# Performance work log

Measured on AMD Instinct MI355X. Metric: run time of the kernel, lower is better.

## Reference

```python
import jax, jax.numpy as jnp
import numpy as np

B, L, C = 2, 2048, 1024
H = 16
D = C // H  # 64
ROPE_THETA = 10000.0


def _rope_tables(seq_len, head_dim, dtype=jnp.float32):
    # freqs_cis equivalent: angle[t, j] = t * theta^(-2j/head_dim)
    inv_freq = 1.0 / (ROPE_THETA ** (jnp.arange(0, head_dim, 2, dtype=jnp.float32) / head_dim))
    ang = jnp.arange(seq_len, dtype=jnp.float32)[:, None] * inv_freq[None, :]  # [L, D/2]
    return jnp.cos(ang).astype(dtype), jnp.sin(ang).astype(dtype)


def setup_inputs() -> dict:
    key = jax.random.key(0)
    k1, k2, k3 = jax.random.split(key, 3)
    x = jax.random.normal(k1, (B, L, C), dtype=jnp.float32)
    qkv_w = jax.random.normal(k2, (3 * C, C), dtype=jnp.float32) * 0.02
    proj_w = jax.random.normal(k3, (C, C), dtype=jnp.float32) * 0.02
    proj_b = jnp.zeros((C,), dtype=jnp.float32)
    cos, sin = _rope_tables(L, D)
    return {"x": x, "qkv_w": qkv_w, "proj_w": proj_w, "proj_b": proj_b, "cos": cos, "sin": sin}


def _apply_rope(t, cos, sin):
    # t: [B, L, H, D]; cos/sin: [L, D/2]; interleaved complex rotation
    te = t[..., 0::2]
    to = t[..., 1::2]
    c = cos[None, :, None, :]
    s = sin[None, :, None, :]
    re = te * c - to * s
    im = te * s + to * c
    out = jnp.stack([re, im], axis=-1)  # [B, L, H, D/2, 2]
    return out.reshape(t.shape)


def reference(x, qkv_w, proj_w, proj_b, cos, sin):
    b, l, c = x.shape
    scale = (c // H) ** -0.5
    qkv = (x @ qkv_w.T).reshape(b, l, 3, H, c // H)  # [B, L, 3, H, D]
    q, k, v = qkv[:, :, 0], qkv[:, :, 1], qkv[:, :, 2]  # each [B, L, H, D]
    q = _apply_rope(q, cos, sin)
    k = _apply_rope(k, cos, sin)
    # memory_efficient_attention math: softmax(q k^T * scale) v, per head
    logits = jnp.einsum("blhd,bmhd->bhlm", q, k) * scale  # [B, H, L, L]
    p = jax.nn.softmax(logits, axis=-1)
    out = jnp.einsum("bhlm,bmhd->blhd", p, v).reshape(b, l, c)
    return out @ proj_w.T + proj_b
```

## Files before the change

### kernel.cpp

```cpp
#include <hip/hip_runtime.h>


typedef __attribute__((ext_vector_type(8))) short s8v;
typedef __attribute__((ext_vector_type(4))) float f4v;

__device__ __forceinline__ unsigned short f2bf(float f) {
  unsigned int u = __float_as_uint(f);
  u += 0x7FFFu + ((u >> 16) & 1u);
  return (unsigned short)(u >> 16);
}

__device__ __forceinline__ void gl16(const unsigned short* g, unsigned short* l) {
  __builtin_amdgcn_global_load_lds((const __attribute__((address_space(1))) void*)g,
                                   (__attribute__((address_space(3))) void*)l,
                                   16, 0, 0);
}

__device__ __forceinline__ s8v pack8(const float* p) {
  const float4 a = *reinterpret_cast<const float4*>(p);
  const float4 b = *reinterpret_cast<const float4*>(p + 4);
  s8v r;
  r[0]=(short)f2bf(a.x); r[1]=(short)f2bf(a.y); r[2]=(short)f2bf(a.z); r[3]=(short)f2bf(a.w);
  r[4]=(short)f2bf(b.x); r[5]=(short)f2bf(b.y); r[6]=(short)f2bf(b.z); r[7]=(short)f2bf(b.w);
  return r;
}

__global__ __launch_bounds__(256)
void k_convert(const float* __restrict__ X, const float* __restrict__ W,
               const float* __restrict__ Wp,
               unsigned short* __restrict__ Xb, unsigned short* __restrict__ Wb,
               unsigned short* __restrict__ Wpb)
{
  const int bid = blockIdx.x, tid = threadIdx.x;
  if (bid < 2048) {
    const size_t e = (size_t)bid * 2048 + (size_t)tid * 8;
    *reinterpret_cast<s8v*>(Xb + e) = pack8(X + e);
  } else if (bid < 3584) {
    const size_t e = (size_t)(bid - 2048) * 2048 + (size_t)tid * 8;
    const int p = (int)(e >> 10);
    const int col = (int)(e & 1023);
    int n;
    if (p < 2048) {
      const int t = p >> 10;
      const int hh = (p & 1023) >> 6;
      const int c = p & 63;
      const int d = (c < 32) ? (c << 1) : (((c - 32) << 1) | 1);
      n = (t << 10) + (hh << 6) + d;
    } else {
      n = p;
    }
    *reinterpret_cast<s8v*>(Wb + e) = pack8(W + (size_t)n * 1024 + col);
  } else {
    const size_t e = (size_t)(bid - 3584) * 2048 + (size_t)tid * 8;
    *reinterpret_cast<s8v*>(Wpb + e) = pack8(Wp + e);
  }
}

__global__ __launch_bounds__(256)
void k_gemm_qkv(const unsigned short* __restrict__ Ab,
                const unsigned short* __restrict__ Bb,
                const float* __restrict__ Ct, const float* __restrict__ St,
                unsigned short* __restrict__ qb, unsigned short* __restrict__ kb,
                unsigned short* __restrict__ vb)
{
  __shared__ __align__(16) unsigned short Asm[128 * 32];
  __shared__ __align__(16) unsigned short Bsm[128 * 32];

  const int tid  = threadIdx.x;
  const int w    = tid >> 6;
  const int lane = tid & 63;
  const int lr   = lane & 15;
  const int lg   = lane >> 4;
  const int wm   = w >> 1, wn = w & 1;

  const int row0 = blockIdx.x << 7;
  const int col0 = blockIdx.y << 7;

  const int srow = (w << 5) + (lane >> 2);
  const int scol = (lane & 3) << 3;
  const unsigned short* Ag = Ab + (size_t)(row0 + srow) * 1024 + scol;
  const unsigned short* Bg = Bb + (size_t)(col0 + srow) * 1024 + scol;
  unsigned short* Al0 = &Asm[(w << 5) * 32];
  unsigned short* Al1 = Al0 + 512;
  unsigned short* Bl0 = &Bsm[(w << 5) * 32];
  unsigned short* Bl1 = Bl0 + 512;

  f4v acc[4][4];
#pragma unroll
  for (int m = 0; m < 4; ++m)
#pragma unroll
    for (int n = 0; n < 4; ++n) acc[m][n] = (f4v){0.f, 0.f, 0.f, 0.f};

  for (int k0 = 0; k0 < 1024; k0 += 32) {
    gl16(Ag + k0, Al0);
    gl16(Ag + k0 + 16 * 1024, Al1);
    gl16(Bg + k0, Bl0);
    gl16(Bg + k0 + 16 * 1024, Bl1);
    __syncthreads();

    s8v af[4], bfr[4];
#pragma unroll
    for (int m = 0; m < 4; ++m)
      af[m] = *reinterpret_cast<const s8v*>(&Asm[(wm * 64 + m * 16 + lr) * 32 + lg * 8]);
#pragma unroll
    for (int n = 0; n < 4; ++n)
      bfr[n] = *reinterpret_cast<const s8v*>(&Bsm[(wn * 64 + n * 16 + lr) * 32 + lg * 8]);
#pragma unroll
    for (int m = 0; m < 4; ++m)
#pragma unroll
      for (int n = 0; n < 4; ++n)
        acc[m][n] = __builtin_amdgcn_mfma_f32_16x16x32_bf16(af[m], bfr[n], acc[m][n], 0, 0, 0);
    __syncthreads();
  }

  const int colbase = col0 + wn * 64;
  const int t  = colbase >> 10;
  const int h  = (colbase & 1023) >> 6;
  unsigned short* dst = (t == 0) ? qb : (t == 1) ? kb : vb;
  const float sc = (t == 0) ? 0.125f : 1.0f;

#pragma unroll
  for (int m = 0; m < 4; ++m) {
#pragma unroll
    for (int j = 0; j < 4; ++j) {
      const int token = row0 + wm * 64 + m * 16 + lg * 4 + j;
      const int bI = token >> 11;
      const int lI = token & 2047;
      unsigned short* rowp = dst + (((size_t)bI * 16 + h) * 2048 + lI) * 64;
      if (t == 2) {
#pragma unroll
        for (int n = 0; n < 4; ++n) rowp[n * 16 + lr] = f2bf(acc[m][n][j]);
      } else {
#pragma unroll
        for (int pn = 0; pn < 2; ++pn) {
          const int d2 = pn * 16 + lr;
          const float c = Ct[lI * 32 + d2];
          const float s = St[lI * 32 + d2];
          const float e = acc[m][pn][j];
          const float o = acc[m][pn + 2][j];
          rowp[d2]      = f2bf((e * c - o * s) * sc);
          rowp[32 + d2] = f2bf((e * s + o * c) * sc);
        }
      }
    }
  }
}

__global__ __launch_bounds__(256)
void k_attn(const unsigned short* __restrict__ qb,
            const unsigned short* __restrict__ kb,
            const unsigned short* __restrict__ vb,
            unsigned short* __restrict__ ab)
{
  __shared__ unsigned short Ps[4][16][72];
  __shared__ unsigned short Vt[64][72];

  const int tid  = threadIdx.x;
  const int w    = tid >> 6;
  const int lane = tid & 63;
  const int lr   = lane & 15;
  const int lg   = lane >> 4;

  const int bx = blockIdx.x;
  const int qt = bx & 31;
  const int h  = (bx >> 5) & 15;
  const int b  = bx >> 9;

  const size_t bh = ((size_t)b * 16 + h) * 2048;
  const unsigned short* Qp = qb + (bh + (size_t)qt * 64 + w * 16) * 64;
  const unsigned short* Kp = kb + bh * 64;
  const unsigned short* Vp = vb + bh * 64;

  const s8v qa0 = *reinterpret_cast<const s8v*>(Qp + lr * 64 + 0 + lg * 8);
  const s8v qa1 = *reinterpret_cast<const s8v*>(Qp + lr * 64 + 32 + lg * 8);

  f4v o[4];
#pragma unroll
  for (int i = 0; i < 4; ++i) o[i] = (f4v){0.f, 0.f, 0.f, 0.f};
  float mrow[4] = {-1e30f, -1e30f, -1e30f, -1e30f};
  float lrow[4] = {0.f, 0.f, 0.f, 0.f};

  const int vc = tid >> 2;
  const int vd = (tid & 3) << 4;

  for (int kt = 0; kt < 32; ++kt) {
    const unsigned short* Kt = Kp + (size_t)kt * 64 * 64;
    const unsigned short* Vs = Vp + (size_t)kt * 64 * 64;

    s8v kf[4][2];
#pragma unroll
    for (int ct = 0; ct < 4; ++ct) {
      kf[ct][0] = *reinterpret_cast<const s8v*>(Kt + (ct * 16 + lr) * 64 + 0 + lg * 8);
      kf[ct][1] = *reinterpret_cast<const s8v*>(Kt + (ct * 16 + lr) * 64 + 32 + lg * 8);
    }
    const s8v v0 = *reinterpret_cast<const s8v*>(Vs + vc * 64 + vd);
    const s8v v1 = *reinterpret_cast<const s8v*>(Vs + vc * 64 + vd + 8);

    __syncthreads();
#pragma unroll
    for (int j = 0; j < 8; ++j) {
      Vt[vd + j][vc]     = (unsigned short)v0[j];
      Vt[vd + 8 + j][vc] = (unsigned short)v1[j];
    }

    f4v s[4];
#pragma unroll
    for (int ct = 0; ct < 4; ++ct) {
      f4v z = (f4v){0.f, 0.f, 0.f, 0.f};
      z = __builtin_amdgcn_mfma_f32_16x16x32_bf16(qa0, kf[ct][0], z, 0, 0, 0);
      z = __builtin_amdgcn_mfma_f32_16x16x32_bf16(qa1, kf[ct][1], z, 0, 0, 0);
      s[ct] = z;
    }

    float pexp[4][4];
#pragma unroll
    for (int r = 0; r < 4; ++r) {
      float mx = fmaxf(fmaxf(s[0][r], s[1][r]), fmaxf(s[2][r], s[3][r]));
#pragma unroll
      for (int mk = 1; mk <= 8; mk <<= 1) mx = fmaxf(mx, __shfl_xor(mx, mk));
      const float mnew = fmaxf(mrow[r], mx);
      const float corr = __expf(mrow[r] - mnew);
      mrow[r] = mnew;
      float rs = 0.f;
#pragma unroll
      for (int ct = 0; ct < 4; ++ct) {
        const float p = __expf(s[ct][r] - mnew);
        pexp[ct][r] = p;
        rs += p;
      }
#pragma unroll
      for (int mk = 1; mk <= 8; mk <<= 1) rs += __shfl_xor(rs, mk);
      lrow[r] = lrow[r] * corr + rs;
      o[0][r] *= corr; o[1][r] *= corr; o[2][r] *= corr; o[3][r] *= corr;
      const int rr = lg * 4 + r;
#pragma unroll
      for (int ct = 0; ct < 4; ++ct)
        Ps[w][rr][ct * 16 + lr] = f2bf(pexp[ct][r]);
    }
    __syncthreads();

    const s8v pa0 = *reinterpret_cast<const s8v*>(&Ps[w][lr][0 + lg * 8]);
    const s8v pa1 = *reinterpret_cast<const s8v*>(&Ps[w][lr][32 + lg * 8]);
#pragma unroll
    for (int dt = 0; dt < 4; ++dt) {
      const s8v vb0 = *reinterpret_cast<const s8v*>(&Vt[dt * 16 + lr][0 + lg * 8]);
      const s8v vb1 = *reinterpret_cast<const s8v*>(&Vt[dt * 16 + lr][32 + lg * 8]);
      o[dt] = __builtin_amdgcn_mfma_f32_16x16x32_bf16(pa0, vb0, o[dt], 0, 0, 0);
      o[dt] = __builtin_amdgcn_mfma_f32_16x16x32_bf16(pa1, vb1, o[dt], 0, 0, 0);
    }
  }

  const int lbase = qt * 64 + w * 16 + lg * 4;
  unsigned short* obase = ab + (size_t)b * 2048 * 1024 + (size_t)h * 64;
#pragma unroll
  for (int r = 0; r < 4; ++r) {
    const float inv = 1.0f / lrow[r];
    unsigned short* orow = obase + (size_t)(lbase + r) * 1024;
    orow[0 + lr]  = f2bf(o[0][r] * inv);
    orow[16 + lr] = f2bf(o[1][r] * inv);
    orow[32 + lr] = f2bf(o[2][r] * inv);
    orow[48 + lr] = f2bf(o[3][r] * inv);
  }
}

__global__ __launch_bounds__(256)
void k_gemm_proj(const unsigned short* __restrict__ Ab,
                 const unsigned short* __restrict__ Bb,
                 const float* __restrict__ PB, float* __restrict__ OUT)
{
  __shared__ __align__(16) unsigned short Asm[128 * 32];
  __shared__ __align__(16) unsigned short Bsm[128 * 32];

  const int tid  = threadIdx.x;
  const int w    = tid >> 6;
  const int lane = tid & 63;
  const int lr   = lane & 15;
  const int lg   = lane >> 4;
  const int wm   = w >> 1, wn = w & 1;

  const int row0 = blockIdx.x << 7;
  const int col0 = blockIdx.y << 7;

  const int srow = (w << 5) + (lane >> 2);
  const int scol = (lane & 3) << 3;
  const unsigned short* Ag = Ab + (size_t)(row0 + srow) * 1024 + scol;
  const unsigned short* Bg = Bb + (size_t)(col0 + srow) * 1024 + scol;
  unsigned short* Al0 = &Asm[(w << 5) * 32];
  unsigned short* Al1 = Al0 + 512;
  unsigned short* Bl0 = &Bsm[(w << 5) * 32];
  unsigned short* Bl1 = Bl0 + 512;

  f4v acc[4][4];
#pragma unroll
  for (int m = 0; m < 4; ++m)
#pragma unroll
    for (int n = 0; n < 4; ++n) acc[m][n] = (f4v){0.f, 0.f, 0.f, 0.f};

  for (int k0 = 0; k0 < 1024; k0 += 32) {
    gl16(Ag + k0, Al0);
    gl16(Ag + k0 + 16 * 1024, Al1);
    gl16(Bg + k0, Bl0);
    gl16(Bg + k0 + 16 * 1024, Bl1);
    __syncthreads();

    s8v af[4], bfr[4];
#pragma unroll
    for (int m = 0; m < 4; ++m)
      af[m] = *reinterpret_cast<const s8v*>(&Asm[(wm * 64 + m * 16 + lr) * 32 + lg * 8]);
#pragma unroll
    for (int n = 0; n < 4; ++n)
      bfr[n] = *reinterpret_cast<const s8v*>(&Bsm[(wn * 64 + n * 16 + lr) * 32 + lg * 8]);
#pragma unroll
    for (int m = 0; m < 4; ++m)
#pragma unroll
      for (int n = 0; n < 4; ++n)
        acc[m][n] = __builtin_amdgcn_mfma_f32_16x16x32_bf16(af[m], bfr[n], acc[m][n], 0, 0, 0);
    __syncthreads();
  }

  float bias[4];
#pragma unroll
  for (int n = 0; n < 4; ++n) bias[n] = PB[col0 + wn * 64 + n * 16 + lr];

#pragma unroll
  for (int m = 0; m < 4; ++m) {
#pragma unroll
    for (int j = 0; j < 4; ++j) {
      const size_t token = row0 + wm * 64 + m * 16 + lg * 4 + j;
      float* orow = OUT + token * 1024 + col0 + wn * 64 + lr;
#pragma unroll
      for (int n = 0; n < 4; ++n) orow[n * 16] = acc[m][n][j] + bias[n];
    }
  }
}

extern "C" void kernel_launch(void* const* d_in, const int* in_sizes, int n_in,
                              void* d_out, int out_size, void* d_ws, size_t ws_size,
                              hipStream_t stream) {
  const float* X    = (const float*)d_in[0];
  const float* Wqkv = (const float*)d_in[1];
  const float* Wp   = (const float*)d_in[2];
  const float* Pb   = (const float*)d_in[3];
  const float* Ct   = (const float*)d_in[4];
  const float* St   = (const float*)d_in[5];
  float* OUT = (float*)d_out;

  unsigned short* Xb  = (unsigned short*)d_ws;
  unsigned short* Wb  = Xb + (size_t)4194304;
  unsigned short* Wpb = Wb + (size_t)3145728;
  unsigned short* qb  = Wpb + (size_t)1048576;
  unsigned short* kb  = qb + (size_t)4194304;
  unsigned short* vb  = kb + (size_t)4194304;
  unsigned short* ab  = vb + (size_t)4194304;

  k_convert<<<dim3(4096), 256, 0, stream>>>(X, Wqkv, Wp, Xb, Wb, Wpb);
  k_gemm_qkv<<<dim3(32, 24), 256, 0, stream>>>(Xb, Wb, Ct, St, qb, kb, vb);
  k_attn<<<dim3(1024), 256, 0, stream>>>(qb, kb, vb, ab);
  k_gemm_proj<<<dim3(32, 8), 256, 0, stream>>>(ab, Wpb, Pb, OUT);
}
```

Baseline: 302.2 us.

## Store V transposed from QKV GEMM and drop LDS transpose in attention

The QKV GEMM epilogue now writes V in a [b,h,d,token] layout using packed 4-element stores. The attention kernel then loads V fragments directly from global memory instead of staging and transposing them through shared memory. This removes the per-tile scalar LDS transpose and both block-wide barriers in the key loop. In exchange, each wave issues its own global V loads, with reuse left to the caches, and the GEMM epilogue writes with a 4 KB stride across rows.

```diff
diff --git a/kernel.cpp b/kernel.cpp
--- a/kernel.cpp
+++ b/kernel.cpp
@@ -3,6 +3,7 @@
 
 typedef __attribute__((ext_vector_type(8))) short s8v;
 typedef __attribute__((ext_vector_type(4))) float f4v;
+typedef __attribute__((ext_vector_type(4))) unsigned short u16x4;
 
 __device__ __forceinline__ unsigned short f2bf(float f) {
   unsigned int u = __float_as_uint(f);
@@ -61,7 +62,7 @@
                 const unsigned short* __restrict__ Bb,
                 const float* __restrict__ Ct, const float* __restrict__ St,
                 unsigned short* __restrict__ qb, unsigned short* __restrict__ kb,
-                unsigned short* __restrict__ vb)
+                unsigned short* __restrict__ vt)
 {
   __shared__ __align__(16) unsigned short Asm[128 * 32];
   __shared__ __align__(16) unsigned short Bsm[128 * 32];
@@ -116,21 +117,34 @@
   const int colbase = col0 + wn * 64;
   const int t  = colbase >> 10;
   const int h  = (colbase & 1023) >> 6;
-  unsigned short* dst = (t == 0) ? qb : (t == 1) ? kb : vb;
-  const float sc = (t == 0) ? 0.125f : 1.0f;
-
-#pragma unroll
-  for (int m = 0; m < 4; ++m) {
-#pragma unroll
-    for (int j = 0; j < 4; ++j) {
-      const int token = row0 + wm * 64 + m * 16 + lg * 4 + j;
+
+  if (t == 2) {
+#pragma unroll
+    for (int m = 0; m < 4; ++m) {
+      const int token = row0 + wm * 64 + m * 16 + lg * 4;
       const int bI = token >> 11;
       const int lI = token & 2047;
-      unsigned short* rowp = dst + (((size_t)bI * 16 + h) * 2048 + lI) * 64;
-      if (t == 2) {
-#pragma unroll
-        for (int n = 0; n < 4; ++n) rowp[n * 16 + lr] = f2bf(acc[m][n][j]);
-      } else {
+      unsigned short* vbase = vt + (((size_t)bI * 16 + h) * 64) * 2048 + lI;
+#pragma unroll
+      for (int n = 0; n < 4; ++n) {
+        const int d = n * 16 + lr;
+        u16x4 pk;
+        pk[0] = f2bf(acc[m][n][0]); pk[1] = f2bf(acc[m][n][1]);
+        pk[2] = f2bf(acc[m][n][2]); pk[3] = f2bf(acc[m][n][3]);
+        *reinterpret_cast<u16x4*>(vbase + (size_t)d * 2048) = pk;
+      }
+    }
+  } else {
+    unsigned short* dst = (t == 0) ? qb : kb;
+    const float sc = (t == 0) ? 0.125f : 1.0f;
+#pragma unroll
+    for (int m = 0; m < 4; ++m) {
+#pragma unroll
+      for (int j = 0; j < 4; ++j) {
+        const int token = row0 + wm * 64 + m * 16 + lg * 4 + j;
+        const int bI = token >> 11;
+        const int lI = token & 2047;
+        unsigned short* rowp = dst + (((size_t)bI * 16 + h) * 2048 + lI) * 64;
 #pragma unroll
         for (int pn = 0; pn < 2; ++pn) {
           const int d2 = pn * 16 + lr;
@@ -149,11 +163,10 @@
 __global__ __launch_bounds__(256)
 void k_attn(const unsigned short* __restrict__ qb,
             const unsigned short* __restrict__ kb,
-            const unsigned short* __restrict__ vb,
+            const unsigned short* __restrict__ vt,
             unsigned short* __restrict__ ab)
 {
   __shared__ unsigned short Ps[4][16][72];
-  __shared__ unsigned short Vt[64][72];
 
   const int tid  = threadIdx.x;
   const int w    = tid >> 6;
@@ -169,7 +182,7 @@
   const size_t bh = ((size_t)b * 16 + h) * 2048;
   const unsigned short* Qp = qb + (bh + (size_t)qt * 64 + w * 16) * 64;
   const unsigned short* Kp = kb + bh * 64;
-  const unsigned short* Vp = vb + bh * 64;
+  const unsigned short* Vtg = vt + bh * 64;
 
   const s8v qa0 = *reinterpret_cast<const s8v*>(Qp + lr * 64 + 0 + lg * 8);
   const s8v qa1 = *reinterpret_cast<const s8v*>(Qp + lr * 64 + 32 + lg * 8);
@@ -180,27 +193,14 @@
   float mrow[4] = {-1e30f, -1e30f, -1e30f, -1e30f};
   float lrow[4] = {0.f, 0.f, 0.f, 0.f};
 
-  const int vc = tid >> 2;
-  const int vd = (tid & 3) << 4;
-
   for (int kt = 0; kt < 32; ++kt) {
     const unsigned short* Kt = Kp + (size_t)kt * 64 * 64;
-    const unsigned short* Vs = Vp + (size_t)kt * 64 * 64;
 
     s8v kf[4][2];
 #pragma unroll
     for (int ct = 0; ct < 4; ++ct) {
       kf[ct][0] = *reinterpret_cast<const s8v*>(Kt + (ct * 16 + lr) * 64 + 0 + lg * 8);
       kf[ct][1] = *reinterpret_cast<const s8v*>(Kt + (ct * 16 + lr) * 64 + 32 + lg * 8);
-    }
-    const s8v v0 = *reinterpret_cast<const s8v*>(Vs + vc * 64 + vd);
-    const s8v v1 = *reinterpret_cast<const s8v*>(Vs + vc * 64 + vd + 8);
-
-    __syncthreads();
-#pragma unroll
-    for (int j = 0; j < 8; ++j) {
-      Vt[vd + j][vc]     = (unsigned short)v0[j];
-      Vt[vd + 8 + j][vc] = (unsigned short)v1[j];
     }
 
     f4v s[4];
@@ -237,14 +237,14 @@
       for (int ct = 0; ct < 4; ++ct)
         Ps[w][rr][ct * 16 + lr] = f2bf(pexp[ct][r]);
     }
-    __syncthreads();
 
     const s8v pa0 = *reinterpret_cast<const s8v*>(&Ps[w][lr][0 + lg * 8]);
     const s8v pa1 = *reinterpret_cast<const s8v*>(&Ps[w][lr][32 + lg * 8]);
 #pragma unroll
     for (int dt = 0; dt < 4; ++dt) {
-      const s8v vb0 = *reinterpret_cast<const s8v*>(&Vt[dt * 16 + lr][0 + lg * 8]);
-      const s8v vb1 = *reinterpret_cast<const s8v*>(&Vt[dt * 16 + lr][32 + lg * 8]);
+      const unsigned short* vrow = Vtg + (size_t)(dt * 16 + lr) * 2048 + kt * 64;
+      const s8v vb0 = *reinterpret_cast<const s8v*>(vrow + lg * 8);
+      const s8v vb1 = *reinterpret_cast<const s8v*>(vrow + 32 + lg * 8);
       o[dt] = __builtin_amdgcn_mfma_f32_16x16x32_bf16(pa0, vb0, o[dt], 0, 0, 0);
       o[dt] = __builtin_amdgcn_mfma_f32_16x16x32_bf16(pa1, vb1, o[dt], 0, 0, 0);
     }
@@ -350,11 +350,11 @@
   unsigned short* Wpb = Wb + (size_t)3145728;
   unsigned short* qb  = Wpb + (size_t)1048576;
   unsigned short* kb  = qb + (size_t)4194304;
-  unsigned short* vb  = kb + (size_t)4194304;
-  unsigned short* ab  = vb + (size_t)4194304;
+  unsigned short* vt  = kb + (size_t)4194304;
+  unsigned short* ab  = vt + (size_t)4194304;
 
   k_convert<<<dim3(4096), 256, 0, stream>>>(X, Wqkv, Wp, Xb, Wb, Wpb);
-  k_gemm_qkv<<<dim3(32, 24), 256, 0, stream>>>(Xb, Wb, Ct, St, qb, kb, vb);
-  k_attn<<<dim3(1024), 256, 0, stream>>>(qb, kb, vb, ab);
+  k_gemm_qkv<<<dim3(32, 24), 256, 0, stream>>>(Xb, Wb, Ct, St, qb, kb, vt);
+  k_attn<<<dim3(1024), 256, 0, stream>>>(qb, kb, vt, ab);
   k_gemm_proj<<<dim3(32, 8), 256, 0, stream>>>(ab, Wpb, Pb, OUT);
 }
```

Result: slower. 382.5 us (+26.6%).
